# Performance work log

Hardware: AMD Instinct MI355X
Metric: run time of the kernel (lower is better)

Reference implementation:

```python
import jax, jax.numpy as jnp
import numpy as np

B, S, L, H, D, DF = 2, 1024, 2, 8, 512, 2048
DK = D // H  # head dim (dk == dv == 64)
EPS = 1e-5


def _ln(x, g, b):
    m = jnp.mean(x, axis=-1, keepdims=True)
    v = jnp.mean((x - m) ** 2, axis=-1, keepdims=True)
    return (x - m) / jnp.sqrt(v + EPS) * g + b


def setup_inputs() -> dict:
    key = jax.random.key(0)
    ks = jax.random.split(key, 8)
    sd = 1.0 / np.sqrt(D)
    sf = 1.0 / np.sqrt(DF)
    inp = {
        "src": jax.random.normal(ks[0], (B, S, D), jnp.float32),
        "Wq": jax.random.normal(ks[1], (L, D, D), jnp.float32) * sd,
        "bq": jnp.zeros((L, D), jnp.float32),
        "Wk": jax.random.normal(ks[2], (L, D, D), jnp.float32) * sd,
        "bk": jnp.zeros((L, D), jnp.float32),
        "Wv": jax.random.normal(ks[3], (L, D, D), jnp.float32) * sd,
        "bv": jnp.zeros((L, D), jnp.float32),
        "Wo": jax.random.normal(ks[4], (L, D, D), jnp.float32) * sd,
        "bo": jnp.zeros((L, D), jnp.float32),
        "W1": jax.random.normal(ks[5], (L, D, DF), jnp.float32) * sd,
        "b1": jnp.zeros((L, DF), jnp.float32),
        "W2": jax.random.normal(ks[6], (L, DF, D), jnp.float32) * sf,
        "b2": jnp.zeros((L, D), jnp.float32),
        "g1": jnp.ones((L, D), jnp.float32),
        "be1": jnp.zeros((L, D), jnp.float32),
        "g2": jnp.ones((L, D), jnp.float32),
        "be2": jnp.zeros((L, D), jnp.float32),
        "gf": jnp.ones((D,), jnp.float32),
        "bef": jnp.zeros((D,), jnp.float32),
    }
    return inp


def _heads(x):
    # [B,S,D] -> [B,H,S,DK]
    return x.reshape(B, S, H, DK).transpose(0, 2, 1, 3)


def _causal_linear_attention(q, k, v):
    # Faithful to torch: cumsum of per-step KV outer products, then query contraction.
    kv = jnp.einsum("bhsk,bhsv->bhskv", k, v)      # [B,H,S,DK,DK]
    cum = jnp.cumsum(kv, axis=2)                     # prefix sums over sequence
    return jnp.einsum("bhsk,bhskv->bhsv", q, cum)   # [B,H,S,DK]


def reference(src, Wq, bq, Wk, bk, Wv, bv, Wo, bo, W1, b1, W2, b2,
              g1, be1, g2, be2, gf, bef):
    x = src
    for i in range(L):
        q = _heads(x @ Wq[i] + bq[i])
        k = _heads(x @ Wk[i] + bk[i])
        v = _heads(x @ Wv[i] + bv[i])
        att = _causal_linear_attention(q, k, v)
        att = att.transpose(0, 2, 1, 3).reshape(B, S, D)
        att = att @ Wo[i] + bo[i]
        x = _ln(x + att, g1[i], be1[i])              # post-norm (normalize_before=False)
        ff = jax.nn.relu(x @ W1[i] + b1[i]) @ W2[i] + b2[i]
        x = _ln(x + ff, g2[i], be2[i])
    return _ln(x, gf, bef)                            # final encoder LayerNorm
```

## Files before the change

### kernel.cpp

```cpp
#include <hip/hip_runtime.h>
#include <hip/hip_bf16.h>

#define DEV static __device__ __forceinline__

typedef __attribute__((ext_vector_type(8))) short short8;
typedef __attribute__((ext_vector_type(4))) float f32x4;

DEV unsigned short f2b(float f){
  unsigned int u = __float_as_uint(f);
  return (unsigned short)((u + 0x7FFFu + ((u >> 16) & 1u)) >> 16);
}
DEV float b2f(unsigned short h){ return __uint_as_float(((unsigned int)h) << 16); }
DEV float load_in(const void* p, size_t i, int isbf){
  return isbf ? b2f(((const unsigned short*)p)[i]) : ((const float*)p)[i];
}
DEV void load_lds16(const unsigned short* g, unsigned short* l){
  __builtin_amdgcn_global_load_lds(
      (const __attribute__((address_space(1))) void*)g,
      (__attribute__((address_space(3))) void*)l, 16, 0, 0);
}

DEV int detect_isbf_block(const void* src){
  __shared__ int cnt[4];
  int tid = threadIdx.x;
  float v = b2f(((const unsigned short*)src)[2 * tid]);
  float av = fabsf(v);
  bool sane = ((av < 64.0f) && (av > 9.5e-7f)) || (v == 0.0f);
  unsigned long long m = __ballot(sane);
  if ((tid & 63) == 0) cnt[tid >> 6] = __popcll(m);
  __syncthreads();
  int tot = cnt[0] + cnt[1] + cnt[2] + cnt[3];
  __syncthreads();
  return tot > 128;
}

struct WDesc { const void* src; long src_off; unsigned short* dst; int K; int N; int tstart; };
struct SDesc { const void* src; int src_off; int dstart; };
struct IngestParams {
  WDesc w[12];
  SDesc s[22];
  float* sdst; int stotal;
  const void* src;
  float* xf; unsigned short* xb;
};

__global__ __launch_bounds__(256) void ingest_all(IngestParams P){
  __shared__ float tile[32][33];
  int b = blockIdx.x, tid = threadIdx.x;
  int isbf = detect_isbf_block(P.src);
  if (b < 6144){
    int t = 0;
    #pragma unroll
    for (int i = 1; i < 12; ++i) if (b >= P.w[i].tstart) t = i;
    WDesc d = P.w[t];
    int r = b - d.tstart;
    int tiles_x = d.N >> 5;
    int tx = r % tiles_x, ty = r / tiles_x;
    int lx = tid & 31, ly = tid >> 5;
    #pragma unroll
    for (int i = 0; i < 4; ++i){
      int row = ty*32 + ly + i*8;
      int col = tx*32 + lx;
      tile[ly + i*8][lx] = load_in(d.src, (size_t)d.src_off + (size_t)row*d.N + col, isbf);
    }
    __syncthreads();
    #pragma unroll
    for (int i = 0; i < 4; ++i){
      int orow = tx*32 + ly + i*8;
      int ocol = ty*32 + lx;
      d.dst[(size_t)orow*d.K + ocol] = f2b(tile[lx][ly + i*8]);
    }
    return;
  }
  int mb = b - 6144;
  if (mb < 4096){
    int i = mb*256 + tid;
    float v = load_in(P.src, (size_t)i, isbf);
    P.xf[i] = v; P.xb[i] = f2b(v);
  } else {
    int i = (mb - 4096)*256 + tid;
    if (i < P.stotal){
      int t = 0;
      #pragma unroll
      for (int j = 1; j < 22; ++j) if (i >= P.s[j].dstart) t = j;
      P.sdst[i] = load_in(P.s[t].src, (size_t)P.s[t].src_off + (i - P.s[t].dstart), isbf);
    }
  }
}

struct GemmArgs {
  const unsigned short* A;
  const unsigned short* Bt;
  const float* bias;
  float* Cf;
  unsigned short* Cb;
  int K;
  int lda, ldb, ldc;
  int cshift, cmask;
  size_t cstride;
  size_t cfz;
  int relu;
};

template<int BN>
__global__ __launch_bounds__(256) void gemm_bt(GemmArgs g){
  constexpr int NI = (BN == 128) ? 4 : 2;
  constexpr int NJ = 4;
  constexpr int BPASS = BN / 32;
  __shared__ __align__(16) unsigned short sA[2][128*64];
  __shared__ __align__(16) unsigned short sB[2][BN*64];
  int tid = threadIdx.x;
  int koff = blockIdx.z * g.K;
  int K = g.K, lda = g.lda, ldb = g.ldb;
  size_t bm = (size_t)blockIdx.y * 128, bn = (size_t)blockIdx.x * BN;
  int lane = tid & 63, wv = tid >> 6, quad = lane >> 4, l16 = lane & 15;
  int wm = (BN == 128) ? (wv >> 1) * 64 : wv * 32;
  int wn = (BN == 128) ? (wv & 1) * 64 : 0;
  f32x4 acc[NI][NJ];
  #pragma unroll
  for (int i=0;i<NI;++i)
    #pragma unroll
    for (int j=0;j<NJ;++j) acc[i][j] = (f32x4){0.f,0.f,0.f,0.f};
  int srow = tid >> 3;
  int schunk = (tid & 7) ^ (srow & 7);
  const unsigned short* Ap = g.A  + (bm + srow)*lda + koff + schunk*8;
  const unsigned short* Bp = g.Bt + (bn + srow)*ldb + koff + schunk*8;

  #define STAGE(buf, ko)                                                      \
    do {                                                                      \
      _Pragma("unroll")                                                       \
      for (int p = 0; p < 4; ++p)                                             \
        load_lds16(Ap + (size_t)(p*32)*lda + (ko), &sA[buf][p*2048 + tid*8]); \
      _Pragma("unroll")                                                       \
      for (int p = 0; p < BPASS; ++p)                                         \
        load_lds16(Bp + (size_t)(p*32)*ldb + (ko), &sB[buf][p*2048 + tid*8]); \
    } while (0)

  STAGE(0, 0);
  asm volatile("s_waitcnt vmcnt(0)" ::: "memory");
  __builtin_amdgcn_s_barrier();

  int nt = K >> 6;
  int cur = 0;
  for (int t = 0; t < nt; ++t){
    if (t + 1 < nt){
      STAGE(cur ^ 1, (t + 1) * 64);
      __builtin_amdgcn_sched_barrier(0);
    }
    #pragma unroll
    for (int kk = 0; kk < 2; ++kk){
      short8 af[NI], bfv[NJ];
      #pragma unroll
      for (int i=0;i<NI;++i){
        int row = wm + i*16 + l16;
        int ch  = (kk*4 + quad) ^ (row & 7);
        af[i] = *(const short8*)&sA[cur][row*64 + ch*8];
      }
      #pragma unroll
      for (int j=0;j<NJ;++j){
        int row = wn + j*16 + l16;
        int ch  = (kk*4 + quad) ^ (row & 7);
        bfv[j] = *(const short8*)&sB[cur][row*64 + ch*8];
      }
      #pragma unroll
      for (int i=0;i<NI;++i)
        #pragma unroll
        for (int j=0;j<NJ;++j)
          acc[i][j] = __builtin_amdgcn_mfma_f32_16x16x32_bf16(af[i], bfv[j], acc[i][j], 0,0,0);
    }
    if (t + 1 < nt){
      asm volatile("s_waitcnt vmcnt(0)" ::: "memory");
      __builtin_amdgcn_s_barrier();
    }
    cur ^= 1;
  }
  #undef STAGE

  float* Cf = g.Cf ? g.Cf + (size_t)blockIdx.z * g.cfz : nullptr;
  unsigned short* Cb = g.Cb;
  #pragma unroll
  for (int j=0;j<NJ;++j){
    int col = (int)bn + wn + j*16 + l16;
    float bv = g.bias ? g.bias[col] : 0.f;
    size_t cbase = ((size_t)(col >> g.cshift))*g.cstride + (col & g.cmask);
    #pragma unroll
    for (int i=0;i<NI;++i){
      #pragma unroll
      for (int r=0;r<4;++r){
        int row = (int)bm + wm + i*16 + quad*4 + r;
        float v = acc[i][j][r] + bv;
        if (g.relu) v = fmaxf(v, 0.f);
        size_t idx = cbase + (size_t)row*g.ldc;
        if (Cf) Cf[idx] = v;
        if (Cb) Cb[idx] = f2b(v);
      }
    }
  }
}

#define ATT_S 1024
#define ATT_D 512

__global__ __launch_bounds__(256) void attn_state_kernel(
    const unsigned short* k, const unsigned short* v, float* states)
{
  __shared__ __align__(16) unsigned short sVt[64*72];
  __shared__ __align__(16) unsigned short sKt[64*72];
  int tid = threadIdx.x;
  int c = blockIdx.x, bh = blockIdx.y;
  int b = bh >> 3, h = bh & 7;
  const size_t base = ((size_t)b*ATT_S + (size_t)c*64)*ATT_D + h*64;
  int lane = tid & 63, wv = tid >> 6, quad = lane >> 4, l16 = lane & 15;

  int t = lane, vc = wv*8;
  const unsigned short* vp = v + base + (size_t)t*ATT_D;
  const unsigned short* kp = k + base + (size_t)t*ATT_D;
  float4 v0 = *(const float4*)(vp + vc);
  float4 v1 = *(const float4*)(vp + vc + 32);
  float4 k0 = *(const float4*)(kp + vc);
  float4 k1 = *(const float4*)(kp + vc + 32);
  {
    const unsigned short* pv0 = (const unsigned short*)&v0;
    const unsigned short* pv1 = (const unsigned short*)&v1;
    const unsigned short* pk0 = (const unsigned short*)&k0;
    const unsigned short* pk1 = (const unsigned short*)&k1;
    #pragma unroll
    for (int e = 0; e < 8; ++e){
      sVt[(vc+e)*72 + t]    = pv0[e];
      sVt[(vc+32+e)*72 + t] = pv1[e];
      sKt[(vc+e)*72 + t]    = pk0[e];
      sKt[(vc+32+e)*72 + t] = pk1[e];
    }
  }
  __syncthreads();

  f32x4 acc[4];
  #pragma unroll
  for (int j=0;j<4;++j) acc[j] = (f32x4){0.f,0.f,0.f,0.f};
  #pragma unroll
  for (int kk=0;kk<2;++kk){
    short8 a = *(const short8*)&sVt[(wv*16 + l16)*72 + kk*32 + quad*8];
    #pragma unroll
    for (int j=0;j<4;++j){
      short8 bb = *(const short8*)&sKt[(j*16 + l16)*72 + kk*32 + quad*8];
      acc[j] = __builtin_amdgcn_mfma_f32_16x16x32_bf16(a, bb, acc[j], 0,0,0);
    }
  }
  float* st = states + ((size_t)bh*16 + c)*4096;
  #pragma unroll
  for (int j=0;j<4;++j)
    #pragma unroll
    for (int rr=0;rr<4;++rr)
      st[(wv*16 + quad*4 + rr)*64 + j*16 + l16] = acc[j][rr];
}

__global__ __launch_bounds__(256) void attn_out_kernel(
    const unsigned short* q, const unsigned short* k, const unsigned short* v,
    const float* states, unsigned short* att)
{
  __shared__ __align__(16) unsigned short sQ [64*72];
  __shared__ __align__(16) unsigned short sK [64*72];
  __shared__ __align__(16) unsigned short sVt[64*72];
  __shared__ __align__(16) float sKV[64*68];
  int tid = threadIdx.x;
  int c = blockIdx.x, bh = blockIdx.y;
  int b = bh >> 3, h = bh & 7;
  const size_t base = ((size_t)b*ATT_S + (size_t)c*64)*ATT_D + h*64;
  int lane = tid & 63, wv = tid >> 6, quad = lane >> 4, l16 = lane & 15;

  float4 racc[4];
  #pragma unroll
  for (int u=0;u<4;++u) racc[u] = (float4){0.f,0.f,0.f,0.f};
  const float* sbase = states + (size_t)bh*16*4096;
  for (int cc = 0; cc < c; ++cc){
    const float4* sp = (const float4*)(sbase + (size_t)cc*4096);
    #pragma unroll
    for (int u=0;u<4;++u){
      float4 t4 = sp[tid + u*256];
      racc[u].x += t4.x; racc[u].y += t4.y; racc[u].z += t4.z; racc[u].w += t4.w;
    }
  }
  #pragma unroll
  for (int u=0;u<4;++u){
    int e = (tid + u*256)*4;
    int row = e >> 6, col = e & 63;
    *(float4*)&sKV[row*68 + col] = racc[u];
  }

  int r = tid >> 2, c8 = (tid & 3)*8;
  const unsigned short* qp = q + base + (size_t)r*ATT_D;
  const unsigned short* kp = k + base + (size_t)r*ATT_D;
  float4 q0 = *(const float4*)(qp + c8);
  float4 q1 = *(const float4*)(qp + c8 + 32);
  float4 k0 = *(const float4*)(kp + c8);
  float4 k1 = *(const float4*)(kp + c8 + 32);
  int t = lane, vc = wv*8;
  const unsigned short* vp = v + base + (size_t)t*ATT_D;
  float4 v0 = *(const float4*)(vp + vc);
  float4 v1 = *(const float4*)(vp + vc + 32);
  *(float4*)&sQ[r*72 + c8]      = q0;
  *(float4*)&sQ[r*72 + c8 + 32] = q1;
  *(float4*)&sK[r*72 + c8]      = k0;
  *(float4*)&sK[r*72 + c8 + 32] = k1;
  {
    const unsigned short* pv0 = (const unsigned short*)&v0;
    const unsigned short* pv1 = (const unsigned short*)&v1;
    #pragma unroll
    for (int e=0;e<8;++e){
      sVt[(vc+e)*72 + t]    = pv0[e];
      sVt[(vc+32+e)*72 + t] = pv1[e];
    }
  }
  __syncthreads();

  f32x4 accS[4];
  #pragma unroll
  for (int j=0;j<4;++j) accS[j] = (f32x4){0.f,0.f,0.f,0.f};
  #pragma unroll
  for (int kk=0;kk<2;++kk){
    short8 a = *(const short8*)&sQ[(wv*16 + l16)*72 + kk*32 + quad*8];
    #pragma unroll
    for (int j=0;j<4;++j){
      short8 bb = *(const short8*)&sK[(j*16 + l16)*72 + kk*32 + quad*8];
      accS[j] = __builtin_amdgcn_mfma_f32_16x16x32_bf16(a, bb, accS[j], 0,0,0);
    }
  }
  __syncthreads();

  #pragma unroll
  for (int j=0;j<4;++j)
    #pragma unroll
    for (int rr=0;rr<4;++rr){
      int i  = wv*16 + quad*4 + rr;
      int cj = j*16 + l16;
      sK[i*72 + cj] = f2b((i >= cj) ? accS[j][rr] : 0.f);
    }

  f32x4 accO[4];
  #pragma unroll
  for (int j=0;j<4;++j) accO[j] = (f32x4){0.f,0.f,0.f,0.f};
  #pragma unroll
  for (int kk=0;kk<2;++kk){
    short8 a = *(const short8*)&sQ[(wv*16 + l16)*72 + kk*32 + quad*8];
    #pragma unroll
    for (int j=0;j<4;++j){
      const float* pf = &sKV[(j*16 + l16)*68 + kk*32 + quad*8];
      short8 bb;
      #pragma unroll
      for (int e=0;e<8;++e) ((unsigned short*)&bb)[e] = f2b(pf[e]);
      accO[j] = __builtin_amdgcn_mfma_f32_16x16x32_bf16(a, bb, accO[j], 0,0,0);
    }
  }
  __syncthreads();

  #pragma unroll
  for (int kk=0;kk<2;++kk){
    short8 a = *(const short8*)&sK[(wv*16 + l16)*72 + kk*32 + quad*8];
    #pragma unroll
    for (int j=0;j<4;++j){
      short8 bb = *(const short8*)&sVt[(j*16 + l16)*72 + kk*32 + quad*8];
      accO[j] = __builtin_amdgcn_mfma_f32_16x16x32_bf16(a, bb, accO[j], 0,0,0);
    }
  }
  #pragma unroll
  for (int j=0;j<4;++j)
    #pragma unroll
    for (int rr=0;rr<4;++rr){
      int i  = wv*16 + quad*4 + rr;
      int cj = j*16 + l16;
      att[base + (size_t)i*ATT_D + cj] = f2b(accO[j][rr]);
    }
}

__global__ __launch_bounds__(256) void add_ln_kernel(
    const float* x, const float* p, int np, const float* bias,
    const float* g, const float* bta,
    float* outf, unsigned short* outb, void* outd, const void* dsrc, int rows)
{
  int isbf = 0;
  if (dsrc) isbf = detect_isbf_block(dsrc);
  int row = blockIdx.x*4 + (threadIdx.x >> 6);
  int lane = threadIdx.x & 63;
  if (row >= rows) return;
  const float* xr = x + (size_t)row*512;
  float a[8];
  *(float4*)&a[0] = *(const float4*)(xr + lane*4);
  *(float4*)&a[4] = *(const float4*)(xr + 256 + lane*4);
  for (int s = 0; s < np; ++s){
    const float* pr = p + (size_t)s*1048576 + (size_t)row*512;
    float yb[8];
    *(float4*)&yb[0] = *(const float4*)(pr + lane*4);
    *(float4*)&yb[4] = *(const float4*)(pr + 256 + lane*4);
    #pragma unroll
    for (int e=0;e<8;++e) a[e] += yb[e];
  }
  if (bias){
    float bb2[8];
    *(float4*)&bb2[0] = *(const float4*)(bias + lane*4);
    *(float4*)&bb2[4] = *(const float4*)(bias + 256 + lane*4);
    #pragma unroll
    for (int e=0;e<8;++e) a[e] += bb2[e];
  }
  float s = 0.f, qq = 0.f;
  #pragma unroll
  for (int e=0;e<8;++e){ s += a[e]; qq += a[e]*a[e]; }
  #pragma unroll
  for (int off=32; off>0; off>>=1){
    s  += __shfl_xor(s,  off, 64);
    qq += __shfl_xor(qq, off, 64);
  }
  float mean = s * (1.f/512.f);
  float var  = qq * (1.f/512.f) - mean*mean;
  float rstd = rsqrtf(var + 1e-5f);
  float gg[8], bb[8];
  *(float4*)&gg[0] = *(const float4*)(g + lane*4);
  *(float4*)&gg[4] = *(const float4*)(g + 256 + lane*4);
  *(float4*)&bb[0] = *(const float4*)(bta + lane*4);
  *(float4*)&bb[4] = *(const float4*)(bta + 256 + lane*4);
  #pragma unroll
  for (int e=0;e<8;++e) a[e] = (a[e]-mean)*rstd*gg[e] + bb[e];
  if (outf){
    float* orow = outf + (size_t)row*512;
    *(float4*)(orow + lane*4)       = *(float4*)&a[0];
    *(float4*)(orow + 256 + lane*4) = *(float4*)&a[4];
  }
  if (outb){
    unsigned short* orow = outb + (size_t)row*512;
    #pragma unroll
    for (int e=0;e<4;++e){ orow[lane*4+e] = f2b(a[e]); orow[256+lane*4+e] = f2b(a[4+e]); }
  }
  if (outd){
    if (isbf){
      unsigned short* od = (unsigned short*)outd + (size_t)row*512;
      #pragma unroll
      for (int e=0;e<4;++e){ od[lane*4+e] = f2b(a[e]); od[256+lane*4+e] = f2b(a[4+e]); }
    } else {
      float* od = (float*)outd + (size_t)row*512;
      *(float4*)(od + lane*4)       = *(float4*)&a[0];
      *(float4*)(od + 256 + lane*4) = *(float4*)&a[4];
    }
  }
}

extern "C" void kernel_launch(void* const* d_in, const int* in_sizes, int n_in,
                              void* d_out, int out_size, void* d_ws, size_t ws_size,
                              hipStream_t stream)
{
  (void)in_sizes; (void)n_in; (void)out_size; (void)ws_size;
  const void* src = d_in[0];
  const void* Wq = d_in[1];  const void* bq = d_in[2];
  const void* Wk = d_in[3];  const void* bk = d_in[4];
  const void* Wv = d_in[5];  const void* bv = d_in[6];
  const void* Wo = d_in[7];  const void* bo = d_in[8];
  const void* W1 = d_in[9];  const void* b1 = d_in[10];
  const void* W2 = d_in[11]; const void* b2 = d_in[12];
  const void* g1 = d_in[13]; const void* be1 = d_in[14];
  const void* g2 = d_in[15]; const void* be2 = d_in[16];
  const void* gf = d_in[17]; const void* bef = d_in[18];

  char* W = (char*)d_ws;
  float* smalls          = (float*)(W + 256);
  unsigned short* wt     = (unsigned short*)(W + 65536);
  float* x_f             = (float*)(W + 12648448);
  unsigned short* x_b    = (unsigned short*)(W + 16842752);
  unsigned short* q_b    = (unsigned short*)(W + 18939904);
  unsigned short* att_b  = (unsigned short*)(W + 25231360);
  float* pp              = (float*)(W + 27328512);
  unsigned short* h1_b   = (unsigned short*)(W + 44105728);
  float* states          = (float*)(W + 44105728);
  unsigned short* k_b = q_b + 1048576;
  unsigned short* v_b = q_b + 2097152;

  IngestParams ip;
  {
    const void* wsrc[6] = {Wq, Wk, Wv, Wo, W1, W2};
    int wK[6] = {512,512,512,512,512,2048};
    int wN[6] = {512,512,512,512,2048,512};
    long wsz[6] = {262144,262144,262144,262144,1048576,1048576};
    int tstart = 0; size_t dsto = 0;
    for (int l=0;l<2;++l)
      for (int ti=0;ti<6;++ti){
        int idx = l*6+ti;
        ip.w[idx].src = wsrc[ti];
        ip.w[idx].src_off = (long)l * wsz[ti];
        ip.w[idx].dst = wt + dsto;
        ip.w[idx].K = wK[ti]; ip.w[idx].N = wN[ti];
        ip.w[idx].tstart = tstart;
        tstart += (wK[ti]/32)*(wN[ti]/32);
        dsto += (size_t)wsz[ti];
      }
    const void* ss[10] = {bq,bk,bv,bo,b1,b2,g1,be1,g2,be2};
    int slen[10] = {512,512,512,512,2048,512,512,512,512,512};
    int dcur = 0, di = 0;
    for (int l=0;l<2;++l)
      for (int ti=0;ti<10;++ti){
        ip.s[di].src = ss[ti];
        ip.s[di].src_off = l * slen[ti];
        ip.s[di].dstart = dcur;
        dcur += slen[ti]; ++di;
      }
    ip.s[20].src = gf;  ip.s[20].src_off = 0; ip.s[20].dstart = dcur; dcur += 512;
    ip.s[21].src = bef; ip.s[21].src_off = 0; ip.s[21].dstart = dcur; dcur += 512;
    ip.sdst = smalls; ip.stotal = dcur;
    ip.src = src; ip.xf = x_f; ip.xb = x_b;
    ingest_all<<<dim3(10296), 256, 0, stream>>>(ip);
  }

  for (int l = 0; l < 2; ++l){
    unsigned short* WqkvT = wt + (size_t)l*3145728;
    unsigned short* WoT   = WqkvT + 786432;
    unsigned short* W1T   = WqkvT + 1048576;
    unsigned short* W2T   = WqkvT + 2097152;
    float* base  = smalls + l*6656;
    float* p_bqkv= base;
    float* p_bo  = base + 1536;
    float* p_b1  = base + 2048;
    float* p_b2  = base + 4096;
    float* p_g1  = base + 4608;
    float* p_be1 = base + 5120;
    float* p_g2  = base + 5632;
    float* p_be2 = base + 6144;

    GemmArgs qkv = {};
    qkv.A = x_b; qkv.Bt = WqkvT; qkv.bias = p_bqkv;
    qkv.Cf = nullptr; qkv.Cb = q_b;
    qkv.K = 512; qkv.lda = 512; qkv.ldb = 512; qkv.ldc = 512;
    qkv.cshift = 9; qkv.cmask = 511; qkv.cstride = 1048576; qkv.cfz = 0; qkv.relu = 0;
    gemm_bt<64><<<dim3(24,16,1), 256, 0, stream>>>(qkv);

    attn_state_kernel<<<dim3(16,16), 256, 0, stream>>>(k_b, v_b, states);
    attn_out_kernel<<<dim3(16,16), 256, 0, stream>>>(q_b, k_b, v_b, states, att_b);

    GemmArgs go = {};
    go.A = att_b; go.Bt = WoT; go.bias = nullptr;
    go.Cf = pp; go.Cb = nullptr;
    go.K = 256; go.lda = 512; go.ldb = 512; go.ldc = 512;
    go.cshift = 30; go.cmask = 0x3fffffff; go.cstride = 0; go.cfz = 1048576; go.relu = 0;
    gemm_bt<64><<<dim3(8,16,2), 256, 0, stream>>>(go);

    add_ln_kernel<<<dim3(512), 256, 0, stream>>>(x_f, pp, 2, p_bo, p_g1, p_be1,
                                                 x_f, x_b, nullptr, nullptr, 2048);

    GemmArgs f1 = {};
    f1.A = x_b; f1.Bt = W1T; f1.bias = p_b1;
    f1.Cf = nullptr; f1.Cb = h1_b;
    f1.K = 512; f1.lda = 512; f1.ldb = 512; f1.ldc = 2048;
    f1.cshift = 30; f1.cmask = 0x3fffffff; f1.cstride = 0; f1.cfz = 0; f1.relu = 1;
    gemm_bt<128><<<dim3(16,16,1), 256, 0, stream>>>(f1);

    GemmArgs f2 = {};
    f2.A = h1_b; f2.Bt = W2T; f2.bias = nullptr;
    f2.Cf = pp; f2.Cb = nullptr;
    f2.K = 1024; f2.lda = 2048; f2.ldb = 2048; f2.ldc = 512;
    f2.cshift = 30; f2.cmask = 0x3fffffff; f2.cstride = 0; f2.cfz = 1048576; f2.relu = 0;
    gemm_bt<64><<<dim3(8,16,2), 256, 0, stream>>>(f2);

    add_ln_kernel<<<dim3(512), 256, 0, stream>>>(x_f, pp, 2, p_b2, p_g2, p_be2,
                                                 x_f, x_b, nullptr, nullptr, 2048);
  }

  add_ln_kernel<<<dim3(512), 256, 0, stream>>>(x_f, nullptr, 0, nullptr,
                                               smalls + 13312, smalls + 13824,
                                               nullptr, nullptr, d_out, src, 2048);
}
```

Measured before the change: 265.9 us.

## Fuse all encoder stages into one persistent kernel with grid barriers

Replaces the sequence of about 17 kernel launches with a single persistent kernel of 256 blocks that runs ingest, QKV GEMM, attention, output GEMM, LayerNorms and the FFN GEMMs, separated by atomic-counter grid barriers. The QKV GEMM now uses 128-wide tiles over 192 blocks, and the final LayerNorm is fused into the last add+LN. The aim is to remove per-launch overhead and tail gaps between small kernels. In exchange, occupancy is fixed at 256 blocks with 64KB of shared memory each, and correctness depends on all blocks being co-resident, since otherwise the spin barrier could deadlock.

After: 927.4 us. +248.8%, slower.

```diff
diff --git a/kernel.cpp b/kernel.cpp
--- a/kernel.cpp
+++ b/kernel.cpp
@@ -20,8 +20,26 @@
       (__attribute__((address_space(3))) void*)l, 16, 0, 0);
 }
 
-DEV int detect_isbf_block(const void* src){
-  __shared__ int cnt[4];
+struct GBar { int gen; int cnt; };
+#define NBLK 256
+
+DEV void grid_sync(GBar* bar, int target){
+  __syncthreads();
+  if (threadIdx.x == 0){
+    __threadfence();
+    int prev = __hip_atomic_fetch_add(&bar->cnt, 1, __ATOMIC_ACQ_REL, __HIP_MEMORY_SCOPE_AGENT);
+    if (prev == NBLK - 1){
+      __hip_atomic_store(&bar->cnt, 0, __ATOMIC_RELAXED, __HIP_MEMORY_SCOPE_AGENT);
+      __hip_atomic_store(&bar->gen, target, __ATOMIC_RELEASE, __HIP_MEMORY_SCOPE_AGENT);
+    } else {
+      while (__hip_atomic_load(&bar->gen, __ATOMIC_ACQUIRE, __HIP_MEMORY_SCOPE_AGENT) < target)
+        __builtin_amdgcn_s_sleep(2);
+    }
+  }
+  __syncthreads();
+}
+
+DEV int detect_isbf(const void* src, int* cnt){
   int tid = threadIdx.x;
   float v = b2f(((const unsigned short*)src)[2 * tid]);
   float av = fabsf(v);
@@ -36,18 +54,26 @@
 
 struct WDesc { const void* src; long src_off; unsigned short* dst; int K; int N; int tstart; };
 struct SDesc { const void* src; int src_off; int dstart; };
-struct IngestParams {
+struct MegaParams {
   WDesc w[12];
   SDesc s[22];
-  float* sdst; int stotal;
+  int stotal;
   const void* src;
+  float* sdst;
+  unsigned short* wt;
   float* xf; unsigned short* xb;
+  unsigned short* qb;
+  unsigned short* attb;
+  float* pp;
+  unsigned short* h1;
+  float* states;
+  GBar* bar;
+  void* dout;
 };
 
-__global__ __launch_bounds__(256) void ingest_all(IngestParams P){
-  __shared__ float tile[32][33];
-  int b = blockIdx.x, tid = threadIdx.x;
-  int isbf = detect_isbf_block(P.src);
+DEV void dev_ingest_unit(const MegaParams& P, int b, int isbf, char* smem){
+  float (*tile)[33] = (float (*)[33])smem;
+  int tid = threadIdx.x;
   if (b < 6144){
     int t = 0;
     #pragma unroll
@@ -70,6 +96,7 @@
       int ocol = ty*32 + lx;
       d.dst[(size_t)orow*d.K + ocol] = f2b(tile[lx][ly + i*8]);
     }
+    __syncthreads();
     return;
   }
   int mb = b - 6144;
@@ -103,16 +130,16 @@
 };
 
 template<int BN>
-__global__ __launch_bounds__(256) void gemm_bt(GemmArgs g){
+DEV void dev_gemm(GemmArgs g, int bxi, int byi, int bzi, char* smem){
   constexpr int NI = (BN == 128) ? 4 : 2;
   constexpr int NJ = 4;
   constexpr int BPASS = BN / 32;
-  __shared__ __align__(16) unsigned short sA[2][128*64];
-  __shared__ __align__(16) unsigned short sB[2][BN*64];
+  unsigned short* sA = (unsigned short*)smem;
+  unsigned short* sB = (unsigned short*)(smem + 32768);
   int tid = threadIdx.x;
-  int koff = blockIdx.z * g.K;
+  int koff = bzi * g.K;
   int K = g.K, lda = g.lda, ldb = g.ldb;
-  size_t bm = (size_t)blockIdx.y * 128, bn = (size_t)blockIdx.x * BN;
+  size_t bm = (size_t)byi * 128, bn = (size_t)bxi * BN;
   int lane = tid & 63, wv = tid >> 6, quad = lane >> 4, l16 = lane & 15;
   int wm = (BN == 128) ? (wv >> 1) * 64 : wv * 32;
   int wn = (BN == 128) ? (wv & 1) * 64 : 0;
@@ -126,14 +153,14 @@
   const unsigned short* Ap = g.A  + (bm + srow)*lda + koff + schunk*8;
   const unsigned short* Bp = g.Bt + (bn + srow)*ldb + koff + schunk*8;
 
-  #define STAGE(buf, ko)                                                      \
-    do {                                                                      \
-      _Pragma("unroll")                                                       \
-      for (int p = 0; p < 4; ++p)                                             \
-        load_lds16(Ap + (size_t)(p*32)*lda + (ko), &sA[buf][p*2048 + tid*8]); \
-      _Pragma("unroll")                                                       \
-      for (int p = 0; p < BPASS; ++p)                                         \
-        load_lds16(Bp + (size_t)(p*32)*ldb + (ko), &sB[buf][p*2048 + tid*8]); \
+  #define STAGE(buf, ko)                                                           \
+    do {                                                                           \
+      _Pragma("unroll")                                                            \
+      for (int p = 0; p < 4; ++p)                                                  \
+        load_lds16(Ap + (size_t)(p*32)*lda + (ko), sA + (buf)*8192 + p*2048 + tid*8); \
+      _Pragma("unroll")                                                            \
+      for (int p = 0; p < BPASS; ++p)                                              \
+        load_lds16(Bp + (size_t)(p*32)*ldb + (ko), sB + (buf)*(BN*64) + p*2048 + tid*8); \
     } while (0)
 
   STAGE(0, 0);
@@ -154,13 +181,13 @@
       for (int i=0;i<NI;++i){
         int row = wm + i*16 + l16;
         int ch  = (kk*4 + quad) ^ (row & 7);
-        af[i] = *(const short8*)&sA[cur][row*64 + ch*8];
+        af[i] = *(const short8*)&sA[cur*8192 + row*64 + ch*8];
       }
       #pragma unroll
       for (int j=0;j<NJ;++j){
         int row = wn + j*16 + l16;
         int ch  = (kk*4 + quad) ^ (row & 7);
-        bfv[j] = *(const short8*)&sB[cur][row*64 + ch*8];
+        bfv[j] = *(const short8*)&sB[cur*(BN*64) + row*64 + ch*8];
       }
       #pragma unroll
       for (int i=0;i<NI;++i)
@@ -176,7 +203,7 @@
   }
   #undef STAGE
 
-  float* Cf = g.Cf ? g.Cf + (size_t)blockIdx.z * g.cfz : nullptr;
+  float* Cf = g.Cf ? g.Cf + (size_t)bzi * g.cfz : nullptr;
   unsigned short* Cb = g.Cb;
   #pragma unroll
   for (int j=0;j<NJ;++j){
@@ -201,13 +228,11 @@
 #define ATT_S 1024
 #define ATT_D 512
 
-__global__ __launch_bounds__(256) void attn_state_kernel(
-    const unsigned short* k, const unsigned short* v, float* states)
-{
-  __shared__ __align__(16) unsigned short sVt[64*72];
-  __shared__ __align__(16) unsigned short sKt[64*72];
+DEV void dev_attn_state(int c, int bh, const unsigned short* k, const unsigned short* v,
+                        float* states, char* smem){
+  unsigned short* sVt = (unsigned short*)smem;
+  unsigned short* sKt = (unsigned short*)(smem + 9216);
   int tid = threadIdx.x;
-  int c = blockIdx.x, bh = blockIdx.y;
   int b = bh >> 3, h = bh & 7;
   const size_t base = ((size_t)b*ATT_S + (size_t)c*64)*ATT_D + h*64;
   int lane = tid & 63, wv = tid >> 6, quad = lane >> 4, l16 = lane & 15;
@@ -254,16 +279,14 @@
       st[(wv*16 + quad*4 + rr)*64 + j*16 + l16] = acc[j][rr];
 }
 
-__global__ __launch_bounds__(256) void attn_out_kernel(
-    const unsigned short* q, const unsigned short* k, const unsigned short* v,
-    const float* states, unsigned short* att)
-{
-  __shared__ __align__(16) unsigned short sQ [64*72];
-  __shared__ __align__(16) unsigned short sK [64*72];
-  __shared__ __align__(16) unsigned short sVt[64*72];
-  __shared__ __align__(16) float sKV[64*68];
+DEV void dev_attn_out(int c, int bh, const unsigned short* q, const unsigned short* k,
+                      const unsigned short* v, const float* states,
+                      unsigned short* att, char* smem){
+  unsigned short* sQ  = (unsigned short*)smem;
+  unsigned short* sK  = (unsigned short*)(smem + 9216);
+  unsigned short* sVt = (unsigned short*)(smem + 18432);
+  float*          sKV = (float*)(smem + 27648);
   int tid = threadIdx.x;
-  int c = blockIdx.x, bh = blockIdx.y;
   int b = bh >> 3, h = bh & 7;
   const size_t base = ((size_t)b*ATT_S + (size_t)c*64)*ATT_D + h*64;
   int lane = tid & 63, wv = tid >> 6, quad = lane >> 4, l16 = lane & 15;
@@ -372,16 +395,12 @@
     }
 }
 
-__global__ __launch_bounds__(256) void add_ln_kernel(
-    const float* x, const float* p, int np, const float* bias,
-    const float* g, const float* bta,
-    float* outf, unsigned short* outb, void* outd, const void* dsrc, int rows)
-{
-  int isbf = 0;
-  if (dsrc) isbf = detect_isbf_block(dsrc);
-  int row = blockIdx.x*4 + (threadIdx.x >> 6);
+DEV void dev_add_ln(int u, const float* x, const float* p, int np, const float* bias,
+                    const float* g, const float* bta,
+                    float* outf, unsigned short* outb, void* outd, int isbf,
+                    const float* g2, const float* b2){
+  int row = u*4 + (threadIdx.x >> 6);
   int lane = threadIdx.x & 63;
-  if (row >= rows) return;
   const float* xr = x + (size_t)row*512;
   float a[8];
   *(float4*)&a[0] = *(const float4*)(xr + lane*4);
@@ -419,6 +438,26 @@
   *(float4*)&bb[4] = *(const float4*)(bta + 256 + lane*4);
   #pragma unroll
   for (int e=0;e<8;++e) a[e] = (a[e]-mean)*rstd*gg[e] + bb[e];
+  if (g2){
+    float s2 = 0.f, q2 = 0.f;
+    #pragma unroll
+    for (int e=0;e<8;++e){ s2 += a[e]; q2 += a[e]*a[e]; }
+    #pragma unroll
+    for (int off=32; off>0; off>>=1){
+      s2 += __shfl_xor(s2, off, 64);
+      q2 += __shfl_xor(q2, off, 64);
+    }
+    float m2 = s2 * (1.f/512.f);
+    float v2 = q2 * (1.f/512.f) - m2*m2;
+    float r2 = rsqrtf(v2 + 1e-5f);
+    float gg2[8], bb22[8];
+    *(float4*)&gg2[0]  = *(const float4*)(g2 + lane*4);
+    *(float4*)&gg2[4]  = *(const float4*)(g2 + 256 + lane*4);
+    *(float4*)&bb22[0] = *(const float4*)(b2 + lane*4);
+    *(float4*)&bb22[4] = *(const float4*)(b2 + 256 + lane*4);
+    #pragma unroll
+    for (int e=0;e<8;++e) a[e] = (a[e]-m2)*r2*gg2[e] + bb22[e];
+  }
   if (outf){
     float* orow = outf + (size_t)row*512;
     *(float4*)(orow + lane*4)       = *(float4*)&a[0];
@@ -438,6 +477,86 @@
       float* od = (float*)outd + (size_t)row*512;
       *(float4*)(od + lane*4)       = *(float4*)&a[0];
       *(float4*)(od + 256 + lane*4) = *(float4*)&a[4];
+    }
+  }
+}
+
+__global__ __launch_bounds__(256) void mega(MegaParams P){
+  __shared__ __align__(16) char smem[65536];
+  int bid = blockIdx.x;
+  int sync_no = 0;
+  int isbf = detect_isbf(P.src, (int*)smem);
+  __syncthreads();
+
+  for (int u = bid; u < 10296; u += NBLK)
+    dev_ingest_unit(P, u, isbf, smem);
+  grid_sync(P.bar, ++sync_no);
+
+  unsigned short* kb = P.qb + 1048576;
+  unsigned short* vb = P.qb + 2097152;
+
+  for (int l = 0; l < 2; ++l){
+    unsigned short* WqkvT = P.wt + (size_t)l*3145728;
+    unsigned short* WoT   = WqkvT + 786432;
+    unsigned short* W1T   = WqkvT + 1048576;
+    unsigned short* W2T   = WqkvT + 2097152;
+    float* base  = P.sdst + l*6656;
+    float* p_bqkv= base;
+    float* p_bo  = base + 1536;
+    float* p_b1  = base + 2048;
+    float* p_b2  = base + 4096;
+    float* p_g1  = base + 4608;
+    float* p_be1 = base + 5120;
+    float* p_g2  = base + 5632;
+    float* p_be2 = base + 6144;
+
+    {
+      GemmArgs a = {P.xb, WqkvT, p_bqkv, nullptr, P.qb, 512, 512, 512, 512,
+                    9, 511, 1048576, 0, 0};
+      if (bid < 192) dev_gemm<128>(a, bid % 12, bid / 12, 0, smem);
+    }
+    grid_sync(P.bar, ++sync_no);
+
+    dev_attn_state(bid & 15, bid >> 4, kb, vb, P.states, smem);
+    grid_sync(P.bar, ++sync_no);
+
+    dev_attn_out(bid & 15, bid >> 4, P.qb, kb, vb, P.states, P.attb, smem);
+    grid_sync(P.bar, ++sync_no);
+
+    {
+      GemmArgs a = {P.attb, WoT, nullptr, P.pp, nullptr, 256, 512, 512, 512,
+                    30, 0x3fffffff, 0, 1048576, 0};
+      dev_gemm<64>(a, bid & 7, (bid >> 3) & 15, bid >> 7, smem);
+    }
+    grid_sync(P.bar, ++sync_no);
+
+    dev_add_ln(bid,        P.xf, P.pp, 2, p_bo, p_g1, p_be1, P.xf, P.xb, nullptr, 0, nullptr, nullptr);
+    dev_add_ln(bid + NBLK, P.xf, P.pp, 2, p_bo, p_g1, p_be1, P.xf, P.xb, nullptr, 0, nullptr, nullptr);
+    grid_sync(P.bar, ++sync_no);
+
+    {
+      GemmArgs a = {P.xb, W1T, p_b1, nullptr, P.h1, 512, 512, 512, 2048,
+                    30, 0x3fffffff, 0, 0, 1};
+      dev_gemm<128>(a, bid & 15, bid >> 4, 0, smem);
+    }
+    grid_sync(P.bar, ++sync_no);
+
+    {
+      GemmArgs a = {P.h1, W2T, nullptr, P.pp, nullptr, 1024, 2048, 2048, 512,
+                    30, 0x3fffffff, 0, 1048576, 0};
+      dev_gemm<64>(a, bid & 7, (bid >> 3) & 15, bid >> 7, smem);
+    }
+    grid_sync(P.bar, ++sync_no);
+
+    if (l == 0){
+      dev_add_ln(bid,        P.xf, P.pp, 2, p_b2, p_g2, p_be2, P.xf, P.xb, nullptr, 0, nullptr, nullptr);
+      dev_add_ln(bid + NBLK, P.xf, P.pp, 2, p_b2, p_g2, p_be2, P.xf, P.xb, nullptr, 0, nullptr, nullptr);
+      grid_sync(P.bar, ++sync_no);
+    } else {
+      const float* p_gf  = P.sdst + 13312;
+      const float* p_bef = P.sdst + 13824;
+      dev_add_ln(bid,        P.xf, P.pp, 2, p_b2, p_g2, p_be2, nullptr, nullptr, P.dout, isbf, p_gf, p_bef);
+      dev_add_ln(bid + NBLK, P.xf, P.pp, 2, p_b2, p_g2, p_be2, nullptr, nullptr, P.dout, isbf, p_gf, p_bef);
     }
   }
 }
@@ -459,19 +578,20 @@
   const void* gf = d_in[17]; const void* bef = d_in[18];
 
   char* W = (char*)d_ws;
-  float* smalls          = (float*)(W + 256);
-  unsigned short* wt     = (unsigned short*)(W + 65536);
-  float* x_f             = (float*)(W + 12648448);
-  unsigned short* x_b    = (unsigned short*)(W + 16842752);
-  unsigned short* q_b    = (unsigned short*)(W + 18939904);
-  unsigned short* att_b  = (unsigned short*)(W + 25231360);
-  float* pp              = (float*)(W + 27328512);
-  unsigned short* h1_b   = (unsigned short*)(W + 44105728);
-  float* states          = (float*)(W + 44105728);
-  unsigned short* k_b = q_b + 1048576;
-  unsigned short* v_b = q_b + 2097152;
-
-  IngestParams ip;
+  MegaParams P;
+  P.src   = src;
+  P.sdst  = (float*)(W + 256);
+  P.wt    = (unsigned short*)(W + 65536);
+  P.xf    = (float*)(W + 12648448);
+  P.xb    = (unsigned short*)(W + 16842752);
+  P.qb    = (unsigned short*)(W + 18939904);
+  P.attb  = (unsigned short*)(W + 25231360);
+  P.pp    = (float*)(W + 27328512);
+  P.h1    = (unsigned short*)(W + 44105728);
+  P.states= (float*)(W + 44105728);
+  P.bar   = (GBar*)(W + 53477376);
+  P.dout  = d_out;
+
   {
     const void* wsrc[6] = {Wq, Wk, Wv, Wo, W1, W2};
     int wK[6] = {512,512,512,512,512,2048};
@@ -481,11 +601,11 @@
     for (int l=0;l<2;++l)
       for (int ti=0;ti<6;++ti){
         int idx = l*6+ti;
-        ip.w[idx].src = wsrc[ti];
-        ip.w[idx].src_off = (long)l * wsz[ti];
-        ip.w[idx].dst = wt + dsto;
-        ip.w[idx].K = wK[ti]; ip.w[idx].N = wN[ti];
-        ip.w[idx].tstart = tstart;
+        P.w[idx].src = wsrc[ti];
+        P.w[idx].src_off = (long)l * wsz[ti];
+        P.w[idx].dst = P.wt + dsto;
+        P.w[idx].K = wK[ti]; P.w[idx].N = wN[ti];
+        P.w[idx].tstart = tstart;
         tstart += (wK[ti]/32)*(wN[ti]/32);
         dsto += (size_t)wsz[ti];
       }
@@ -494,72 +614,16 @@
     int dcur = 0, di = 0;
     for (int l=0;l<2;++l)
       for (int ti=0;ti<10;++ti){
-        ip.s[di].src = ss[ti];
-        ip.s[di].src_off = l * slen[ti];
-        ip.s[di].dstart = dcur;
+        P.s[di].src = ss[ti];
+        P.s[di].src_off = l * slen[ti];
+        P.s[di].dstart = dcur;
         dcur += slen[ti]; ++di;
       }
-    ip.s[20].src = gf;  ip.s[20].src_off = 0; ip.s[20].dstart = dcur; dcur += 512;
-    ip.s[21].src = bef; ip.s[21].src_off = 0; ip.s[21].dstart = dcur; dcur += 512;
-    ip.sdst = smalls; ip.stotal = dcur;
-    ip.src = src; ip.xf = x_f; ip.xb = x_b;
-    ingest_all<<<dim3(10296), 256, 0, stream>>>(ip);
-  }
-
-  for (int l = 0; l < 2; ++l){
-    unsigned short* WqkvT = wt + (size_t)l*3145728;
-    unsigned short* WoT   = WqkvT + 786432;
-    unsigned short* W1T   = WqkvT + 1048576;
-    unsigned short* W2T   = WqkvT + 2097152;
-    float* base  = smalls + l*6656;
-    float* p_bqkv= base;
-    float* p_bo  = base + 1536;
-    float* p_b1  = base + 2048;
-    float* p_b2  = base + 4096;
-    float* p_g1  = base + 4608;
-    float* p_be1 = base + 5120;
-    float* p_g2  = base + 5632;
-    float* p_be2 = base + 6144;
-
-    GemmArgs qkv = {};
-    qkv.A = x_b; qkv.Bt = WqkvT; qkv.bias = p_bqkv;
-    qkv.Cf = nullptr; qkv.Cb = q_b;
-    qkv.K = 512; qkv.lda = 512; qkv.ldb = 512; qkv.ldc = 512;
-    qkv.cshift = 9; qkv.cmask = 511; qkv.cstride = 1048576; qkv.cfz = 0; qkv.relu = 0;
-    gemm_bt<64><<<dim3(24,16,1), 256, 0, stream>>>(qkv);
-
-    attn_state_kernel<<<dim3(16,16), 256, 0, stream>>>(k_b, v_b, states);
-    attn_out_kernel<<<dim3(16,16), 256, 0, stream>>>(q_b, k_b, v_b, states, att_b);
-
-    GemmArgs go = {};
-    go.A = att_b; go.Bt = WoT; go.bias = nullptr;
-    go.Cf = pp; go.Cb = nullptr;
-    go.K = 256; go.lda = 512; go.ldb = 512; go.ldc = 512;
-    go.cshift = 30; go.cmask = 0x3fffffff; go.cstride = 0; go.cfz = 1048576; go.relu = 0;
-    gemm_bt<64><<<dim3(8,16,2), 256, 0, stream>>>(go);
-
-    add_ln_kernel<<<dim3(512), 256, 0, stream>>>(x_f, pp, 2, p_bo, p_g1, p_be1,
-                                                 x_f, x_b, nullptr, nullptr, 2048);
-
-    GemmArgs f1 = {};
-    f1.A = x_b; f1.Bt = W1T; f1.bias = p_b1;
-    f1.Cf = nullptr; f1.Cb = h1_b;
-    f1.K = 512; f1.lda = 512; f1.ldb = 512; f1.ldc = 2048;
-    f1.cshift = 30; f1.cmask = 0x3fffffff; f1.cstride = 0; f1.cfz = 0; f1.relu = 1;
-    gemm_bt<128><<<dim3(16,16,1), 256, 0, stream>>>(f1);
-
-    GemmArgs f2 = {};
-    f2.A = h1_b; f2.Bt = W2T; f2.bias = nullptr;
-    f2.Cf = pp; f2.Cb = nullptr;
-    f2.K = 1024; f2.lda = 2048; f2.ldb = 2048; f2.ldc = 512;
-    f2.cshift = 30; f2.cmask = 0x3fffffff; f2.cstride = 0; f2.cfz = 1048576; f2.relu = 0;
-    gemm_bt<64><<<dim3(8,16,2), 256, 0, stream>>>(f2);
-
-    add_ln_kernel<<<dim3(512), 256, 0, stream>>>(x_f, pp, 2, p_b2, p_g2, p_be2,
-                                                 x_f, x_b, nullptr, nullptr, 2048);
-  }
-
-  add_ln_kernel<<<dim3(512), 256, 0, stream>>>(x_f, nullptr, 0, nullptr,
-                                               smalls + 13312, smalls + 13824,
-                                               nullptr, nullptr, d_out, src, 2048);
-}
+    P.s[20].src = gf;  P.s[20].src_off = 0; P.s[20].dstart = dcur; dcur += 512;
+    P.s[21].src = bef; P.s[21].src_off = 0; P.s[21].dstart = dcur; dcur += 512;
+    P.stotal = dcur;
+  }
+
+  hipMemsetAsync(P.bar, 0, sizeof(GBar), stream);
+  mega<<<dim3(NBLK), 256, 0, stream>>>(P);
+}
```
